# Kernel optimization log

Measured on AMD Instinct MI355X. Metric: run time of the kernel, lower is better.

Reference implementation:

```python
import jax, jax.numpy as jnp
import numpy as np

N = 8192
E = 262144
D_IN = 128
D_OUT = 128

def setup_inputs() -> dict:
    key = jax.random.key(0)
    k1, k2, k3, k4 = jax.random.split(key, 4)
    x = jax.random.normal(k1, (N, D_IN), dtype=jnp.float32)
    edge_index = jax.random.randint(k2, (2, E), 0, N, dtype=jnp.int64)
    W = jax.random.normal(k3, (D_OUT, D_IN), dtype=jnp.float32) * 0.05
    b = jax.random.normal(k4, (D_OUT,), dtype=jnp.float32) * 0.05
    return {"x": x, "edge_index": edge_index, "W": W, "b": b}

def reference(x, edge_index, W, b):
    num_nodes = x.shape[0]
    # Dense adjacency: adj[src, dst] = 1.0 (duplicate edges set, not add)
    adj = jnp.zeros((num_nodes, num_nodes), dtype=x.dtype)
    adj = adj.at[edge_index[0], edge_index[1]].set(1.0)
    adj = adj + jnp.eye(num_nodes, dtype=x.dtype)  # self-loops (added on top)
    degree = adj.sum(axis=1, keepdims=True)
    degree = jnp.where(degree > 0, degree, jnp.ones_like(degree))
    adj = adj / degree  # row-normalize
    out = adj @ x               # [N, D_IN] aggregation
    out = out @ W.T + b         # nn.Linear
    return out
```

## Files before the change

### kernel.cpp

```cpp
#include <hip/hip_runtime.h>


typedef unsigned int uint32;

#define NNODES 8192
#define DF 128
#define WPR 256
#define M 4
#define CAP 384

__global__ void edge_scatter(const int* __restrict__ ei, int E,
                             uint32* __restrict__ bm) {
    int e = blockIdx.x * blockDim.x + threadIdx.x;
    if (e >= E) return;
    int src = ei[e];
    int dst = ei[E + e];
    atomicOr(&bm[(size_t)src * WPR + (dst >> 5)], 1u << (dst & 31));
}

__global__ __launch_bounds__(128) void gcn_fused(
    const float* __restrict__ x,
    const uint32* __restrict__ bm,
    const float* __restrict__ W,
    const float* __restrict__ b,
    float* __restrict__ out)
{
    __shared__ int   nbr[M][CAP];
    __shared__ int   total[M];
    __shared__ float agg[M][DF];

    const int t = threadIdx.x;
    const int node0 = blockIdx.x * M;

    if (t < M) total[t] = 0;
    __syncthreads();

    for (int m = 0; m < M; ++m) {
        const uint32* r = bm + (size_t)(node0 + m) * WPR;
        uint32 w0 = r[2 * t];
        uint32 w1 = r[2 * t + 1];
        int c = __popc(w0) + __popc(w1);
        if (c) {
            int off = atomicAdd(&total[m], c);
            int base0 = (2 * t) << 5, base1 = (2 * t + 1) << 5;
            while (w0) {
                int bit = __ffs(w0) - 1; w0 &= w0 - 1;
                if (off < CAP) nbr[m][off] = base0 + bit;
                off++;
            }
            while (w1) {
                int bit = __ffs(w1) - 1; w1 &= w1 - 1;
                if (off < CAP) nbr[m][off] = base1 + bit;
                off++;
            }
        }
    }
    __syncthreads();

    float acc[M];
    #pragma unroll
    for (int m = 0; m < M; ++m) acc[m] = x[(size_t)(node0 + m) * DF + t];

    #pragma unroll
    for (int m = 0; m < M; ++m) {
        int cnt = total[m];
        if (cnt <= CAP) {
            int k = 0;
            for (; k + 4 <= cnt; k += 4) {
                int j0 = nbr[m][k], j1 = nbr[m][k + 1],
                    j2 = nbr[m][k + 2], j3 = nbr[m][k + 3];
                float a0 = x[(size_t)j0 * DF + t];
                float a1 = x[(size_t)j1 * DF + t];
                float a2 = x[(size_t)j2 * DF + t];
                float a3 = x[(size_t)j3 * DF + t];
                acc[m] += (a0 + a1) + (a2 + a3);
            }
            for (; k < cnt; ++k) acc[m] += x[(size_t)nbr[m][k] * DF + t];
        } else {
            const uint32* r = bm + (size_t)(node0 + m) * WPR;
            for (int w = 0; w < WPR; ++w) {
                uint32 word = r[w];
                int base = w << 5;
                while (word) {
                    int bit = __ffs(word) - 1; word &= word - 1;
                    acc[m] += x[(size_t)(base + bit) * DF + t];
                }
            }
        }
        agg[m][t] = acc[m] / (float)(1 + cnt);
    }
    __syncthreads();

    const float4* Wrow = (const float4*)(W + (size_t)t * DF);
    float bias = b[t];
    float sum[M];
    #pragma unroll
    for (int m = 0; m < M; ++m) sum[m] = bias;

    #pragma unroll 8
    for (int c4 = 0; c4 < DF / 4; ++c4) {
        float4 wv = Wrow[c4];
        #pragma unroll
        for (int m = 0; m < M; ++m) {
            sum[m] += wv.x * agg[m][c4 * 4 + 0] + wv.y * agg[m][c4 * 4 + 1]
                    + wv.z * agg[m][c4 * 4 + 2] + wv.w * agg[m][c4 * 4 + 3];
        }
    }
    #pragma unroll
    for (int m = 0; m < M; ++m)
        out[(size_t)(node0 + m) * DF + t] = sum[m];
}

extern "C" void kernel_launch(void* const* d_in, const int* in_sizes, int n_in,
                              void* d_out, int out_size, void* d_ws, size_t ws_size,
                              hipStream_t stream) {
    const float* x = (const float*)d_in[0];
    const int*  ei = (const int*)d_in[1];
    const float* W = (const float*)d_in[2];
    const float* b = (const float*)d_in[3];
    float* out = (float*)d_out;

    uint32* bm = (uint32*)d_ws;
    const int E = in_sizes[1] / 2;

    hipMemsetAsync(bm, 0, (size_t)NNODES * WPR * sizeof(uint32), stream);

    edge_scatter<<<dim3((E + 255) / 256), dim3(256), 0, stream>>>(ei, E, bm);
    gcn_fused<<<dim3(NNODES / M), dim3(128), 0, stream>>>(x, bm, W, b, out);
}
```

Measured before the change: 105.6 us.

## Use wave prefix-scan for neighbor lists and float4 gather across neighbor groups

Neighbor list construction now assigns one wavefront per node row, with a shuffle-based prefix scan in place of a shared atomic, producing an ordered list. The gather is restructured so each thread loads float4 chunks while four thread groups split the neighbor list. Lists are padded to a common length using a zero row in workspace so the four nodes are processed together, and partial sums are reduced through shared memory. CAP is halved to cut shared memory, which makes the slow bitmap fallback path more likely for high-degree nodes.

```diff
diff --git a/kernel.cpp b/kernel.cpp
--- a/kernel.cpp
+++ b/kernel.cpp
@@ -7,7 +7,7 @@
 #define DF 128
 #define WPR 256
 #define M 4
-#define CAP 384
+#define CAP 192
 
 __global__ void edge_scatter(const int* __restrict__ ei, int E,
                              uint32* __restrict__ bm) {
@@ -21,73 +21,108 @@
 __global__ __launch_bounds__(128) void gcn_fused(
     const float* __restrict__ x,
     const uint32* __restrict__ bm,
+    const float4* __restrict__ zrow,
     const float* __restrict__ W,
     const float* __restrict__ b,
     float* __restrict__ out)
 {
-    __shared__ int   nbr[M][CAP];
-    __shared__ int   total[M];
+    __shared__ int nbr[M][CAP];
+    __shared__ int cnt_s[M];
+    __shared__ __align__(16) float part[M][4][DF];
     __shared__ float agg[M][DF];
 
-    const int t = threadIdx.x;
+    const int t    = threadIdx.x;
+    const int lane = t & 63;
+    const int wv   = t >> 6;
     const int node0 = blockIdx.x * M;
 
-    if (t < M) total[t] = 0;
-    __syncthreads();
-
-    for (int m = 0; m < M; ++m) {
+    #pragma unroll
+    for (int pass = 0; pass < 2; ++pass) {
+        const int m = pass * 2 + wv;
         const uint32* r = bm + (size_t)(node0 + m) * WPR;
-        uint32 w0 = r[2 * t];
-        uint32 w1 = r[2 * t + 1];
-        int c = __popc(w0) + __popc(w1);
-        if (c) {
-            int off = atomicAdd(&total[m], c);
-            int base0 = (2 * t) << 5, base1 = (2 * t + 1) << 5;
-            while (w0) {
-                int bit = __ffs(w0) - 1; w0 &= w0 - 1;
-                if (off < CAP) nbr[m][off] = base0 + bit;
-                off++;
-            }
-            while (w1) {
-                int bit = __ffs(w1) - 1; w1 &= w1 - 1;
-                if (off < CAP) nbr[m][off] = base1 + bit;
+        uint32 w0 = r[4 * lane + 0], w1 = r[4 * lane + 1],
+               w2 = r[4 * lane + 2], w3 = r[4 * lane + 3];
+        int c = __popc(w0) + __popc(w1) + __popc(w2) + __popc(w3);
+        int v = c;
+        #pragma unroll
+        for (int d = 1; d < 64; d <<= 1) {
+            int up = __shfl_up(v, d);
+            if (lane >= d) v += up;
+        }
+        int off = v - c;
+        if (lane == 63) cnt_s[m] = v;
+        uint32 ws[4] = {w0, w1, w2, w3};
+        #pragma unroll
+        for (int q = 0; q < 4; ++q) {
+            uint32 word = ws[q];
+            int base = (4 * lane + q) << 5;
+            while (word) {
+                int bit = __ffs(word) - 1; word &= word - 1;
+                if (off < CAP) nbr[m][off] = base + bit;
                 off++;
             }
         }
     }
     __syncthreads();
 
-    float acc[M];
-    #pragma unroll
-    for (int m = 0; m < M; ++m) acc[m] = x[(size_t)(node0 + m) * DF + t];
+    const int c0 = cnt_s[0], c1 = cnt_s[1], c2 = cnt_s[2], c3 = cnt_s[3];
+    int Lmax = max(max(c0, c1), max(c2, c3));
+    const bool overflow = (Lmax > CAP);
+    int L = (min(Lmax, CAP) + 3) & ~3;
 
-    #pragma unroll
     for (int m = 0; m < M; ++m) {
-        int cnt = total[m];
-        if (cnt <= CAP) {
-            int k = 0;
-            for (; k + 4 <= cnt; k += 4) {
-                int j0 = nbr[m][k], j1 = nbr[m][k + 1],
-                    j2 = nbr[m][k + 2], j3 = nbr[m][k + 3];
-                float a0 = x[(size_t)j0 * DF + t];
-                float a1 = x[(size_t)j1 * DF + t];
-                float a2 = x[(size_t)j2 * DF + t];
-                float a3 = x[(size_t)j3 * DF + t];
-                acc[m] += (a0 + a1) + (a2 + a3);
+        int cm = min(cnt_s[m], CAP);
+        for (int k = cm + t; k < L; k += 128) nbr[m][k] = -1;
+    }
+    __syncthreads();
+
+    if (!overflow) {
+        const int g = t >> 5;
+        const int c = t & 31;
+        const float4* x4 = (const float4*)x;
+
+        float4 acc[M];
+        #pragma unroll
+        for (int m = 0; m < M; ++m) acc[m] = make_float4(0.f, 0.f, 0.f, 0.f);
+
+        for (int k = g; k < L; k += 4) {
+            #pragma unroll
+            for (int m = 0; m < M; ++m) {
+                int j = nbr[m][k];
+                const float4* p = (j >= 0) ? (x4 + (size_t)j * (DF / 4) + c)
+                                           : (zrow + c);
+                float4 vx = *p;
+                acc[m].x += vx.x; acc[m].y += vx.y;
+                acc[m].z += vx.z; acc[m].w += vx.w;
             }
-            for (; k < cnt; ++k) acc[m] += x[(size_t)nbr[m][k] * DF + t];
-        } else {
+        }
+
+        #pragma unroll
+        for (int m = 0; m < M; ++m)
+            *(float4*)&part[m][g][c * 4] = acc[m];
+        __syncthreads();
+
+        #pragma unroll
+        for (int m = 0; m < M; ++m) {
+            float s = part[m][0][t] + part[m][1][t]
+                    + part[m][2][t] + part[m][3][t];
+            s += x[(size_t)(node0 + m) * DF + t];
+            agg[m][t] = s / (float)(1 + cnt_s[m]);
+        }
+    } else {
+        for (int m = 0; m < M; ++m) {
             const uint32* r = bm + (size_t)(node0 + m) * WPR;
+            float acc = x[(size_t)(node0 + m) * DF + t];
             for (int w = 0; w < WPR; ++w) {
                 uint32 word = r[w];
                 int base = w << 5;
                 while (word) {
                     int bit = __ffs(word) - 1; word &= word - 1;
-                    acc[m] += x[(size_t)(base + bit) * DF + t];
+                    acc += x[(size_t)(base + bit) * DF + t];
                 }
             }
+            agg[m][t] = acc / (float)(1 + cnt_s[m]);
         }
-        agg[m][t] = acc[m] / (float)(1 + cnt);
     }
     __syncthreads();
 
@@ -99,11 +134,11 @@
 
     #pragma unroll 8
     for (int c4 = 0; c4 < DF / 4; ++c4) {
-        float4 wv = Wrow[c4];
+        float4 wvv = Wrow[c4];
         #pragma unroll
         for (int m = 0; m < M; ++m) {
-            sum[m] += wv.x * agg[m][c4 * 4 + 0] + wv.y * agg[m][c4 * 4 + 1]
-                    + wv.z * agg[m][c4 * 4 + 2] + wv.w * agg[m][c4 * 4 + 3];
+            sum[m] += wvv.x * agg[m][c4 * 4 + 0] + wvv.y * agg[m][c4 * 4 + 1]
+                    + wvv.z * agg[m][c4 * 4 + 2] + wvv.w * agg[m][c4 * 4 + 3];
         }
     }
     #pragma unroll
@@ -121,10 +156,12 @@
     float* out = (float*)d_out;
 
     uint32* bm = (uint32*)d_ws;
+    const size_t bm_bytes = (size_t)NNODES * WPR * sizeof(uint32);
+    const float4* zrow = (const float4*)((char*)d_ws + bm_bytes);
     const int E = in_sizes[1] / 2;
 
-    hipMemsetAsync(bm, 0, (size_t)NNODES * WPR * sizeof(uint32), stream);
+    hipMemsetAsync(d_ws, 0, bm_bytes + DF * sizeof(float), stream);
 
     edge_scatter<<<dim3((E + 255) / 256), dim3(256), 0, stream>>>(ei, E, bm);
-    gcn_fused<<<dim3(NNODES / M), dim3(128), 0, stream>>>(x, bm, W, b, out);
+    gcn_fused<<<dim3(NNODES / M), dim3(128), 0, stream>>>(x, bm, zrow, W, b, out);
 }
```

Measured after the change: 100.6 us. 1.05x faster.
